# Kernel tuning notes

Hardware: AMD Instinct MI355X
Metric: run time of the kernel (lower is better)

The kernel has to match this reference:

```python
import jax, jax.numpy as jnp
import numpy as np

EPS = 1e-12  # F.normalize default eps


def setup_inputs() -> dict:
    key = jax.random.key(0)
    ks = jax.random.split(key, 8)
    b, c, h, w = 8, 192, 128, 128
    s = 0.02
    return {
        "x_in": jax.random.normal(ks[0], (b, c, h, w), dtype=jnp.float32),
        "w_split": jax.random.normal(ks[1], (c, c), dtype=jnp.float32) * s,
        "w_q": jax.random.normal(ks[2], (c, c), dtype=jnp.float32) * s,
        "w_k": jax.random.normal(ks[3], (c, c), dtype=jnp.float32) * s,
        "w_v": jax.random.normal(ks[4], (c, c), dtype=jnp.float32) * s,
        "w_proj": jax.random.normal(ks[5], (c, c), dtype=jnp.float32) * s,
        "b_proj": jax.random.normal(ks[6], (c,), dtype=jnp.float32) * s,
        "w_out": jax.random.normal(ks[7], (c, c), dtype=jnp.float32) * s,
    }


def _l2norm(x):
    # F.normalize(p=2, dim=-1): x / max(||x||, eps)
    n = jnp.sqrt(jnp.sum(x * x, axis=-1, keepdims=True))
    return x / jnp.maximum(n, EPS)


def reference(x_in, w_split, w_q, w_k, w_v, w_proj, b_proj, w_out):
    b, c, h, w = x_in.shape
    # conv_split0: 1x1 conv, no bias -> channel matmul
    x = jnp.einsum('oc,bchw->bohw', w_split, x_in)
    # [b,h,w,c] -> [b,hw,c]
    x = x.transpose(0, 2, 3, 1).reshape(b, h * w, c)
    # Linear: y = x @ W^T
    q = jnp.einsum('bnc,oc->bon', x, w_q)  # [b,c,hw] (already transposed)
    k = jnp.einsum('bnc,oc->bon', x, w_k)
    v = jnp.einsum('bnc,oc->bon', x, w_v)
    q = _l2norm(q)
    k = _l2norm(k)
    attn = jax.nn.softmax(jnp.einsum('bcn,bdn->bcd', k, q), axis=-1)  # [b,c,c]
    y = jnp.einsum('bcd,bdn->bcn', attn, v)  # [b,c,hw]
    y = y.transpose(0, 2, 1)  # [b,hw,c]
    out = jnp.einsum('bnc,oc->bno', y, w_proj) + b_proj
    out = out.reshape(b, h, w, c).transpose(0, 3, 1, 2)  # [b,c,h,w]
    out = jnp.einsum('oc,bchw->bohw', w_out, out)
    return out
```

## Files before the change

### kernel.cpp

```cpp
#include <hip/hip_runtime.h>


static constexpr int B_ = 8;
static constexpr int C_ = 192;
static constexpr int N_ = 16384;
static constexpr int CC2 = C_ * C_;
static constexpr int NCHUNK = 32;

using u16x8 = __attribute__((ext_vector_type(8))) unsigned short;
using bf16x8 = __attribute__((ext_vector_type(8))) __bf16;
using f32x4 = __attribute__((ext_vector_type(4))) float;

__device__ __forceinline__ unsigned short f2bf(float f) {
  unsigned int u = __builtin_bit_cast(unsigned int, f);
  u += 0x7FFFu + ((u >> 16) & 1u);
  return (unsigned short)(u >> 16);
}

__device__ __forceinline__ f32x4 mfma16(u16x8 a, u16x8 b, f32x4 c) {
  return __builtin_amdgcn_mfma_f32_16x16x32_bf16(
      __builtin_bit_cast(bf16x8, a), __builtin_bit_cast(bf16x8, b), c, 0, 0, 0);
}

__global__ void fold_kernel(const float* __restrict__ wsplit, const float* __restrict__ wq,
                            const float* __restrict__ wk, const float* __restrict__ wv,
                            const float* __restrict__ wproj, const float* __restrict__ bproj,
                            const float* __restrict__ wout,
                            float* __restrict__ Wq, float* __restrict__ WqT,
                            float* __restrict__ Wk, float* __restrict__ Wv,
                            float* __restrict__ Wo2, float* __restrict__ bias2) {
  int idx = blockIdx.x * 256 + threadIdx.x;
  if (idx < C_) {
    float s = 0.f;
    for (int c = 0; c < C_; ++c) s += wout[idx * C_ + c] * bproj[c];
    bias2[idx] = s;
  }
  if (idx >= 4 * CC2) return;
  int which = idx / CC2;
  int rem = idx % CC2;
  int o = rem / C_, c = rem % C_;
  const float* A = (which == 0) ? wq : (which == 1) ? wk : (which == 2) ? wv : wout;
  const float* Bm = (which == 3) ? wproj : wsplit;
  float s = 0.f;
  for (int e = 0; e < C_; ++e) s += A[o * C_ + e] * Bm[e * C_ + c];
  if (which == 0) { Wq[rem] = s; WqT[c * C_ + o] = s; }
  else if (which == 1) Wk[rem] = s;
  else if (which == 2) Wv[rem] = s;
  else Wo2[rem] = s;
}

template <bool ATOMIC>
__global__ __launch_bounds__(384) void gram3_kernel(const float* __restrict__ xin,
                                                    float* __restrict__ dst) {
  const int b = blockIdx.z, half = blockIdx.y, ch = blockIdx.x;
  const int k0 = ch * 512;
  __shared__ unsigned short Xs[2][C_][72];
  const int tid = threadIdx.x;
  const int wv = tid >> 6;
  const int lane = tid & 63;
  const int ln = lane & 15, mq = lane >> 4;
  const int arow0 = half * 96 + wv * 16;
  const int cbase = tid >> 4;
  const int k4 = tid & 15;
  const float* xb = xin + (size_t)b * C_ * N_;

  f32x4 acc[12];
#pragma unroll
  for (int j = 0; j < 12; ++j) acc[j] = (f32x4)0.0f;

  float4 ld[8];
  auto load_stage = [&](int kbase) {
#pragma unroll
    for (int j = 0; j < 8; ++j)
      ld[j] = *(const float4*)(xb + (size_t)(j * 24 + cbase) * N_ + kbase + k4 * 4);
  };
  auto write_stage = [&](int buf) {
#pragma unroll
    for (int j = 0; j < 8; ++j) {
      unsigned int lo = (unsigned)f2bf(ld[j].x) | ((unsigned)f2bf(ld[j].y) << 16);
      unsigned int hi = (unsigned)f2bf(ld[j].z) | ((unsigned)f2bf(ld[j].w) << 16);
      uint2 pk; pk.x = lo; pk.y = hi;
      *(uint2*)&Xs[buf][j * 24 + cbase][k4 * 4] = pk;
    }
  };

  load_stage(k0);
  write_stage(0);
  __syncthreads();
  for (int s = 0; s < 8; ++s) {
    if (s < 7) load_stage(k0 + (s + 1) * 64);
    const int cb = s & 1;
#pragma unroll
    for (int ks = 0; ks < 2; ++ks) {
      const int kk = ks * 32 + mq * 8;
      u16x8 a0 = *(const u16x8*)&Xs[cb][arow0 + ln][kk];
#pragma unroll
      for (int ct = 0; ct < 12; ++ct) {
        u16x8 bf = *(const u16x8*)&Xs[cb][ct * 16 + ln][kk];
        acc[ct] = mfma16(a0, bf, acc[ct]);
      }
    }
    if (s < 7) {
      write_stage(cb ^ 1);
      __syncthreads();
    }
  }
  float* out = ATOMIC ? dst + (size_t)b * CC2
                      : dst + ((size_t)b * NCHUNK + ch) * CC2;
#pragma unroll
  for (int ct = 0; ct < 12; ++ct)
#pragma unroll
    for (int r = 0; r < 4; ++r) {
      int row = arow0 + mq * 4 + r;
      int col = ct * 16 + ln;
      if (ATOMIC) atomicAdd(&out[row * C_ + col], acc[ct][r]);
      else out[row * C_ + col] = acc[ct][r];
    }
}

__global__ void gsum_kernel(const float* __restrict__ P, float* __restrict__ G) {
  const int j = (blockIdx.x * 256 + threadIdx.x) * 4;
  const int b = blockIdx.y;
  const float* base = P + (size_t)b * NCHUNK * CC2 + j;
  float4 s = {0.f, 0.f, 0.f, 0.f};
#pragma unroll
  for (int ch = 0; ch < NCHUNK; ++ch) {
    float4 v = *(const float4*)(base + (size_t)ch * CC2);
    s.x += v.x; s.y += v.y; s.z += v.z; s.w += v.w;
  }
  *(float4*)(G + (size_t)b * CC2 + j) = s;
}

__global__ __launch_bounds__(192) void tkqn_kernel(const float* __restrict__ Wk,
                                                   const float* __restrict__ Wq,
                                                   const float* __restrict__ G,
                                                   float* __restrict__ Tk,
                                                   float* __restrict__ qn) {
  const int b = blockIdx.y, d = blockIdx.x, t = threadIdx.x;
  const float* Gb = G + (size_t)b * CC2;
  float sk = 0.f, sq = 0.f;
  for (int c = 0; c < C_; ++c) {
    float g = Gb[c * C_ + t];
    sk += Wk[d * C_ + c] * g;
    sq += Wq[d * C_ + c] * g;
  }
  Tk[((size_t)b * C_ + d) * C_ + t] = sk;
  float val = sq * Wq[d * C_ + t];
  __shared__ float red[256];
  red[t] = val;
  if (t < 64) red[192 + t] = 0.f;
  __syncthreads();
  for (int st = 128; st > 0; st >>= 1) {
    if (t < st) red[t] += red[t + st];
    __syncthreads();
  }
  if (t == 0) qn[b * C_ + d] = fmaxf(sqrtf(fmaxf(red[0], 0.f)), 1e-12f);
}

__global__ __launch_bounds__(192) void attn_av_kernel(const float* __restrict__ Tk,
                                                      const float* __restrict__ WqT,
                                                      const float* __restrict__ Wk,
                                                      const float* __restrict__ Wv,
                                                      const float* __restrict__ qn,
                                                      float* __restrict__ Tv) {
  const int b = blockIdx.y, cc = blockIdx.x, t = threadIdx.x;
  __shared__ float tkrow[C_];
  __shared__ float arow[C_];
  __shared__ float red[256];
  tkrow[t] = Tk[((size_t)b * C_ + cc) * C_ + t];
  red[t] = tkrow[t] * Wk[cc * C_ + t];
  if (t < 64) red[192 + t] = 0.f;
  __syncthreads();
  for (int st = 128; st > 0; st >>= 1) {
    if (t < st) red[t] += red[t + st];
    __syncthreads();
  }
  float knv = fmaxf(sqrtf(fmaxf(red[0], 0.f)), 1e-12f);
  __syncthreads();
  float s = 0.f;
  for (int c = 0; c < C_; ++c) s += tkrow[c] * WqT[c * C_ + t];
  float lg = s / (knv * qn[b * C_ + t]);
  red[t] = lg;
  if (t < 64) red[192 + t] = -1e30f;
  __syncthreads();
  for (int st = 128; st > 0; st >>= 1) {
    if (t < st) red[t] = fmaxf(red[t], red[t + st]);
    __syncthreads();
  }
  float mx = red[0];
  __syncthreads();
  float e = expf(lg - mx);
  red[t] = e;
  if (t < 64) red[192 + t] = 0.f;
  __syncthreads();
  for (int st = 128; st > 0; st >>= 1) {
    if (t < st) red[t] += red[t + st];
    __syncthreads();
  }
  float a = e / red[0];
  arow[t] = a;
  __syncthreads();
  float sv = 0.f;
  for (int c = 0; c < C_; ++c) sv += arow[c] * Wv[c * C_ + t];
  Tv[((size_t)b * C_ + cc) * C_ + t] = sv;
}

__global__ void m_kernel(const float* __restrict__ Wo2, const float* __restrict__ Tv,
                         float* __restrict__ Mout) {
  int idx = blockIdx.x * 256 + threadIdx.x;
  if (idx >= B_ * CC2) return;
  int b = idx / CC2;
  int rc = idx % CC2;
  int i = rc / C_, j = rc % C_;
  float s = 0.f;
  for (int c = 0; c < C_; ++c) s += Wo2[i * C_ + c] * Tv[((size_t)b * C_ + c) * C_ + j];
  Mout[idx] = s;
}

__global__ __launch_bounds__(384) void final2_kernel(const float* __restrict__ xin,
                                                     const float* __restrict__ Mw,
                                                     const float* __restrict__ bias2,
                                                     float* __restrict__ out) {
  const int b = blockIdx.y;
  const int p0 = blockIdx.x * 128;
  __shared__ unsigned short Ts[128 * 192];
  const int tid = threadIdx.x;
  const int wv = tid >> 6;
  const int lane = tid & 63;
  const int ln = lane & 15, mq = lane >> 4;
  const float* Mb = Mw + (size_t)b * CC2;

  u16x8 afr[6][2];
  float bo[2][4];
#pragma unroll
  for (int i = 0; i < 2; ++i) {
    int row = 32 * wv + 16 * i + ln;
#pragma unroll
    for (int kc = 0; kc < 6; ++kc) {
      const float* src = Mb + row * C_ + kc * 32 + mq * 8;
      float4 u0 = *(const float4*)(src);
      float4 u1 = *(const float4*)(src + 4);
      u16x8 a;
      a[0] = f2bf(u0.x); a[1] = f2bf(u0.y); a[2] = f2bf(u0.z); a[3] = f2bf(u0.w);
      a[4] = f2bf(u1.x); a[5] = f2bf(u1.y); a[6] = f2bf(u1.z); a[7] = f2bf(u1.w);
      afr[kc][i] = a;
    }
#pragma unroll
    for (int r = 0; r < 4; ++r) bo[i][r] = bias2[32 * wv + 16 * i + mq * 4 + r];
  }

#pragma unroll
  for (int j = 0; j < 16; ++j) {
    int lin = j * 384 + tid;
    int c = lin >> 5, p4 = lin & 31;
    float4 v = *(const float4*)(xin + ((size_t)b * C_ + c) * N_ + p0 + p4 * 4);
#pragma unroll
    for (int jj = 0; jj < 4; ++jj) {
      int e = (jj + (p4 >> 1)) & 3;
      float val = (e == 0) ? v.x : (e == 1) ? v.y : (e == 2) ? v.z : v.w;
      int p = p4 * 4 + e;
      int idx = p * 192 + ((((c >> 3) ^ (p & 7)) << 3) | (c & 7));
      Ts[idx] = f2bf(val);
    }
  }
  __syncthreads();

#pragma unroll
  for (int pt = 0; pt < 8; ++pt) {
    const int p = pt * 16 + ln;
    f32x4 acc0 = (f32x4)0.0f, acc1 = (f32x4)0.0f;
#pragma unroll
    for (int kc = 0; kc < 6; ++kc) {
      u16x8 bf = *(const u16x8*)&Ts[p * 192 + (((kc * 4 + mq) ^ (p & 7)) << 3)];
      acc0 = mfma16(afr[kc][0], bf, acc0);
      acc1 = mfma16(afr[kc][1], bf, acc1);
    }
#pragma unroll
    for (int r = 0; r < 4; ++r) {
      int row0 = 32 * wv + mq * 4 + r;
      int row1 = row0 + 16;
      int pp = p0 + pt * 16 + ln;
      out[((size_t)b * C_ + row0) * N_ + pp] = acc0[r] + bo[0][r];
      out[((size_t)b * C_ + row1) * N_ + pp] = acc1[r] + bo[1][r];
    }
  }
}

extern "C" void kernel_launch(void* const* d_in, const int* in_sizes, int n_in,
                              void* d_out, int out_size, void* d_ws, size_t ws_size,
                              hipStream_t stream) {
  const float* xin    = (const float*)d_in[0];
  const float* wsplit = (const float*)d_in[1];
  const float* wq     = (const float*)d_in[2];
  const float* wk     = (const float*)d_in[3];
  const float* wv     = (const float*)d_in[4];
  const float* wproj  = (const float*)d_in[5];
  const float* bproj  = (const float*)d_in[6];
  const float* wout   = (const float*)d_in[7];
  float* out = (float*)d_out;

  float* ws = (float*)d_ws;
  float* G     = ws;
  float* Wq    = G + (size_t)B_ * CC2;
  float* WqT   = Wq + CC2;
  float* Wk    = WqT + CC2;
  float* Wv    = Wk + CC2;
  float* Wo2   = Wv + CC2;
  float* bias2 = Wo2 + CC2;
  float* Tk    = bias2 + 256;
  float* Tv    = Tk + (size_t)B_ * CC2;
  float* Mw    = Tv + (size_t)B_ * CC2;
  float* qn    = Mw + (size_t)B_ * CC2;
  float* P     = qn + 256 * B_;

  size_t base_floats = (size_t)(P - ws);
  size_t need_bytes = (base_floats + (size_t)B_ * NCHUNK * CC2) * sizeof(float);
  bool use_partials = ws_size >= need_bytes;

  fold_kernel<<<(4 * CC2 + 255) / 256, 256, 0, stream>>>(
      wsplit, wq, wk, wv, wproj, bproj, wout, Wq, WqT, Wk, Wv, Wo2, bias2);
  if (use_partials) {
    gram3_kernel<false><<<dim3(NCHUNK, 2, B_), 384, 0, stream>>>(xin, P);
    gsum_kernel<<<dim3(CC2 / 1024, B_), 256, 0, stream>>>(P, G);
  } else {
    hipMemsetAsync(G, 0, (size_t)B_ * CC2 * sizeof(float), stream);
    gram3_kernel<true><<<dim3(NCHUNK, 2, B_), 384, 0, stream>>>(xin, G);
  }
  tkqn_kernel<<<dim3(C_, B_), 192, 0, stream>>>(Wk, Wq, G, Tk, qn);
  attn_av_kernel<<<dim3(C_, B_), 192, 0, stream>>>(Tk, WqT, Wk, Wv, qn, Tv);
  m_kernel<<<(B_ * CC2 + 255) / 256, 256, 0, stream>>>(Wo2, Tv, Mw);
  final2_kernel<<<dim3(N_ / 128, B_), 384, 0, stream>>>(xin, Mw, bias2, out);
}
```

Before: 325.1 us.

## Halve final GEMM tile and pipeline x staging in two halves

The final kernel now processes 64 pixels per block instead of 128. It loads the second half of the input tile from global memory while computing on the first half, which overlaps loads with MFMA work. Each thread now gathers four channels per pixel and writes packed 8-byte bf16 values to LDS with a revised swizzle, replacing scalar 2-byte stores. Halving the LDS tile and adding a launch-bounds occupancy hint aim to fit more blocks per CU. The cost is that each block reloads and converts the full M fragment set twice as often overall.

```diff
diff --git a/kernel.cpp b/kernel.cpp
--- a/kernel.cpp
+++ b/kernel.cpp
@@ -10,11 +10,22 @@
 using u16x8 = __attribute__((ext_vector_type(8))) unsigned short;
 using bf16x8 = __attribute__((ext_vector_type(8))) __bf16;
 using f32x4 = __attribute__((ext_vector_type(4))) float;
+using uint32x4 = __attribute__((ext_vector_type(4))) unsigned int;
 
 __device__ __forceinline__ unsigned short f2bf(float f) {
   unsigned int u = __builtin_bit_cast(unsigned int, f);
   u += 0x7FFFu + ((u >> 16) & 1u);
   return (unsigned short)(u >> 16);
+}
+
+__device__ __forceinline__ unsigned int pkbf(float lo, float hi) {
+  unsigned short a = __builtin_bit_cast(unsigned short, (__bf16)lo);
+  unsigned short b = __builtin_bit_cast(unsigned short, (__bf16)hi);
+  return (unsigned int)a | ((unsigned int)b << 16);
+}
+
+__device__ __forceinline__ float f4get(const float4& v, int e) {
+  return (e == 0) ? v.x : (e == 1) ? v.y : (e == 2) ? v.z : v.w;
 }
 
 __device__ __forceinline__ f32x4 mfma16(u16x8 a, u16x8 b, f32x4 c) {
@@ -217,19 +228,27 @@
   Mout[idx] = s;
 }
 
-__global__ __launch_bounds__(384) void final2_kernel(const float* __restrict__ xin,
-                                                     const float* __restrict__ Mw,
-                                                     const float* __restrict__ bias2,
-                                                     float* __restrict__ out) {
+__global__ __launch_bounds__(384, 5) void final3_kernel(const float* __restrict__ xin,
+                                                        const float* __restrict__ Mw,
+                                                        const float* __restrict__ bias2,
+                                                        float* __restrict__ out) {
   const int b = blockIdx.y;
-  const int p0 = blockIdx.x * 128;
-  __shared__ unsigned short Ts[128 * 192];
+  const int p0 = blockIdx.x * 64;
+  __shared__ __align__(16) unsigned short Ts[64 * 192];
   const int tid = threadIdx.x;
   const int wv = tid >> 6;
   const int lane = tid & 63;
   const int ln = lane & 15, mq = lane >> 4;
   const float* Mb = Mw + (size_t)b * CC2;
 
+  const int c0 = (tid >> 3) * 4;
+  const int pq = tid & 7;
+  const float* xsrc = xin + ((size_t)b * C_ + c0) * N_ + p0 + pq * 4;
+
+  float4 ldA[4], ldB[4];
+#pragma unroll
+  for (int l = 0; l < 4; ++l) ldA[l] = *(const float4*)(xsrc + (size_t)l * N_);
+
   u16x8 afr[6][2];
   float bo[2][4];
 #pragma unroll
@@ -240,50 +259,56 @@
       const float* src = Mb + row * C_ + kc * 32 + mq * 8;
       float4 u0 = *(const float4*)(src);
       float4 u1 = *(const float4*)(src + 4);
-      u16x8 a;
-      a[0] = f2bf(u0.x); a[1] = f2bf(u0.y); a[2] = f2bf(u0.z); a[3] = f2bf(u0.w);
-      a[4] = f2bf(u1.x); a[5] = f2bf(u1.y); a[6] = f2bf(u1.z); a[7] = f2bf(u1.w);
-      afr[kc][i] = a;
+      uint32x4 w;
+      w[0] = pkbf(u0.x, u0.y); w[1] = pkbf(u0.z, u0.w);
+      w[2] = pkbf(u1.x, u1.y); w[3] = pkbf(u1.z, u1.w);
+      afr[kc][i] = __builtin_bit_cast(u16x8, w);
     }
 #pragma unroll
     for (int r = 0; r < 4; ++r) bo[i][r] = bias2[32 * wv + 16 * i + mq * 4 + r];
   }
 
-#pragma unroll
-  for (int j = 0; j < 16; ++j) {
-    int lin = j * 384 + tid;
-    int c = lin >> 5, p4 = lin & 31;
-    float4 v = *(const float4*)(xin + ((size_t)b * C_ + c) * N_ + p0 + p4 * 4);
-#pragma unroll
-    for (int jj = 0; jj < 4; ++jj) {
-      int e = (jj + (p4 >> 1)) & 3;
-      float val = (e == 0) ? v.x : (e == 1) ? v.y : (e == 2) ? v.z : v.w;
-      int p = p4 * 4 + e;
-      int idx = p * 192 + ((((c >> 3) ^ (p & 7)) << 3) | (c & 7));
-      Ts[idx] = f2bf(val);
-    }
-  }
-  __syncthreads();
-
-#pragma unroll
-  for (int pt = 0; pt < 8; ++pt) {
+  auto stage_write = [&](const float4* ld, int sbase) {
+#pragma unroll
+    for (int e = 0; e < 4; ++e) {
+      int p = sbase + pq * 4 + e;
+      int idx = p * 192 + ((((c0 >> 3) ^ ((p >> 1) & 7)) << 3) | (c0 & 7));
+      uint2 pk;
+      pk.x = pkbf(f4get(ld[0], e), f4get(ld[1], e));
+      pk.y = pkbf(f4get(ld[2], e), f4get(ld[3], e));
+      *(uint2*)&Ts[idx] = pk;
+    }
+  };
+
+  auto compute = [&](int pt) {
     const int p = pt * 16 + ln;
+    const int pkey = (p >> 1) & 7;
     f32x4 acc0 = (f32x4)0.0f, acc1 = (f32x4)0.0f;
 #pragma unroll
     for (int kc = 0; kc < 6; ++kc) {
-      u16x8 bf = *(const u16x8*)&Ts[p * 192 + (((kc * 4 + mq) ^ (p & 7)) << 3)];
+      u16x8 bf = *(const u16x8*)&Ts[p * 192 + (((kc * 4 + mq) ^ pkey) << 3)];
       acc0 = mfma16(afr[kc][0], bf, acc0);
       acc1 = mfma16(afr[kc][1], bf, acc1);
     }
+    const int pp = p0 + p;
 #pragma unroll
     for (int r = 0; r < 4; ++r) {
       int row0 = 32 * wv + mq * 4 + r;
-      int row1 = row0 + 16;
-      int pp = p0 + pt * 16 + ln;
       out[((size_t)b * C_ + row0) * N_ + pp] = acc0[r] + bo[0][r];
-      out[((size_t)b * C_ + row1) * N_ + pp] = acc1[r] + bo[1][r];
-    }
-  }
+      out[((size_t)b * C_ + row0 + 16) * N_ + pp] = acc1[r] + bo[1][r];
+    }
+  };
+
+  stage_write(ldA, 0);
+  __syncthreads();
+#pragma unroll
+  for (int l = 0; l < 4; ++l) ldB[l] = *(const float4*)(xsrc + 32 + (size_t)l * N_);
+  compute(0);
+  compute(1);
+  stage_write(ldB, 32);
+  __syncthreads();
+  compute(2);
+  compute(3);
 }
 
 extern "C" void kernel_launch(void* const* d_in, const int* in_sizes, int n_in,
@@ -329,5 +354,5 @@
   tkqn_kernel<<<dim3(C_, B_), 192, 0, stream>>>(Wk, Wq, G, Tk, qn);
   attn_av_kernel<<<dim3(C_, B_), 192, 0, stream>>>(Tk, WqT, Wk, Wv, qn, Tv);
   m_kernel<<<(B_ * CC2 + 255) / 256, 256, 0, stream>>>(Wo2, Tv, Mw);
-  final2_kernel<<<dim3(N_ / 128, B_), 384, 0, stream>>>(xin, Mw, bias2, out);
-}
+  final3_kernel<<<dim3(N_ / 64, B_), 384, 0, stream>>>(xin, Mw, bias2, out);
+}
```

Result: slower. 417.3 us (+28.4%).
